# Kernel tuning notes

Measured on AMD Instinct MI355X. Metric: run time of the kernel, lower is better.

The kernel has to match this reference:

```python
import jax, jax.numpy as jnp
import numpy as np

N_NODES = 50000
N_EDGES = 800000
IN_C, HID_C, OUT_C = 256, 256, 128


def gcn_conv(x, W, b, row, col, n_nodes):
    """PyG GCNConv: linear transform, symmetric-normalized aggregation, bias.
    row/col already include self-loops. Messages flow row -> col."""
    h = x @ W  # [N, out]
    deg = jax.ops.segment_sum(jnp.ones_like(col, dtype=h.dtype), col, num_segments=n_nodes)
    d_inv_sqrt = jnp.where(deg > 0, jax.lax.rsqrt(jnp.maximum(deg, 1e-12)), 0.0)
    norm = d_inv_sqrt[row] * d_inv_sqrt[col]  # [E]
    msg = h[row] * norm[:, None]              # gather + scale, [E, out]
    out = jax.ops.segment_sum(msg, col, num_segments=n_nodes)  # scatter-add
    return out + b


def setup_inputs() -> dict:
    key = jax.random.key(0)
    k_x, k_e, k_w1, k_w2 = jax.random.split(key, 4)
    x = jax.random.normal(k_x, (N_NODES, IN_C), dtype=jnp.float32)
    edge_index = jax.random.randint(k_e, (2, N_EDGES), 0, N_NODES, dtype=jnp.int64)
    # Glorot-style init for GCN weights, zeros bias (PyG default)
    s1 = float(np.sqrt(6.0 / (IN_C + HID_C)))
    s2 = float(np.sqrt(6.0 / (HID_C + OUT_C)))
    W1 = jax.random.uniform(k_w1, (IN_C, HID_C), dtype=jnp.float32, minval=-s1, maxval=s1)
    b1 = jnp.zeros((HID_C,), dtype=jnp.float32)
    W2 = jax.random.uniform(k_w2, (HID_C, OUT_C), dtype=jnp.float32, minval=-s2, maxval=s2)
    b2 = jnp.zeros((OUT_C,), dtype=jnp.float32)
    return {"x": x, "edge_index": edge_index, "W1": W1, "b1": b1, "W2": W2, "b2": b2}


def reference(x, edge_index, W1, b1, W2, b2):
    n = x.shape[0]
    # add self-loops (PyG GCNConv default add_self_loops=True)
    loops = jnp.arange(n, dtype=edge_index.dtype)
    row = jnp.concatenate([edge_index[0], loops])
    col = jnp.concatenate([edge_index[1], loops])
    h = gcn_conv(x, W1, b1, row, col, n)
    h = jax.nn.relu(h)  # dropout p=0.0 -> identity
    out = gcn_conv(h, W2, b2, row, col, n)
    return out
```

## Files before the change

### kernel.cpp

```cpp
#include <hip/hip_runtime.h>

#define NN 50000
#define NE 800000
#define IN_C 256
#define HID_C 256
#define OUT_C 128

typedef unsigned short u16;
typedef __attribute__((ext_vector_type(8))) short short8;
typedef __attribute__((ext_vector_type(8))) unsigned short ushort8;
typedef __attribute__((ext_vector_type(4))) float f32x4;

__device__ __forceinline__ u16 f2b(float f) {
  unsigned int u = __float_as_uint(f);
  return (u16)((u + 0x7FFFu + ((u >> 16) & 1u)) >> 16);
}
__device__ __forceinline__ float b2f(u16 s) {
  return __uint_as_float(((unsigned int)s) << 16);
}


__global__ __launch_bounds__(256) void convw_zero(const float* __restrict__ W1,
                                                  const float* __restrict__ W2,
                                                  u16* __restrict__ W1t,
                                                  u16* __restrict__ W2t,
                                                  int* __restrict__ cnt) {
  int b = blockIdx.x;
  if (b < 256) {
    int id = b * 256 + threadIdx.x;
    if (id < 256 * 256) {
      int n = id >> 8, k = id & 255;
      W1t[id] = f2b(W1[k * 256 + n]);
    }
    if (id < 128 * 256) {
      int n = id >> 8, k = id & 255;
      W2t[id] = f2b(W2[k * 128 + n]);
    }
  } else {
    int i = (b - 256) * 256 + threadIdx.x;
    if (i < NN) cnt[i] = 0;
  }
}


__global__ __launch_bounds__(256) void hist_kernel(const int* __restrict__ col,
                                                   int* __restrict__ cnt, int E) {
  int e = blockIdx.x * blockDim.x + threadIdx.x;
  if (e < E) atomicAdd(&cnt[col[e]], 1);
}

__global__ __launch_bounds__(256) void scan1_kernel(const int* __restrict__ cnt,
                                                    int* __restrict__ bsum, int n) {
  __shared__ int ws[4];
  int i = blockIdx.x * 256 + threadIdx.x;
  int lane = threadIdx.x & 63, wid = threadIdx.x >> 6;
  int v = (i < n) ? cnt[i] : 0;
#pragma unroll
  for (int off = 32; off > 0; off >>= 1) v += __shfl_down(v, off, 64);
  if (lane == 0) ws[wid] = v;
  __syncthreads();
  if (threadIdx.x == 0) bsum[blockIdx.x] = ws[0] + ws[1] + ws[2] + ws[3];
}

__global__ __launch_bounds__(256) void scan2_kernel(const int* __restrict__ bsum,
                                                    int* __restrict__ boff,
                                                    int* __restrict__ row_off,
                                                    int nb, int n) {
  __shared__ int wsum[4], wpre[5];
  int lane = threadIdx.x & 63, wid = threadIdx.x >> 6;
  int v = (threadIdx.x < nb) ? bsum[threadIdx.x] : 0;
  int s = v;
#pragma unroll
  for (int off = 1; off < 64; off <<= 1) {
    int t = __shfl_up(s, off, 64);
    if (lane >= off) s += t;
  }
  if (lane == 63) wsum[wid] = s;
  __syncthreads();
  if (threadIdx.x == 0) {
    int acc = 0;
#pragma unroll
    for (int w = 0; w < 4; ++w) { wpre[w] = acc; acc += wsum[w]; }
    wpre[4] = acc;
  }
  __syncthreads();
  if (threadIdx.x < nb) boff[threadIdx.x] = wpre[wid] + (s - v);
  if (threadIdx.x == 0) row_off[n] = wpre[4];
}

__global__ __launch_bounds__(256) void scan3_kernel(const int* __restrict__ cnt,
                                                    const int* __restrict__ boff,
                                                    int* __restrict__ row_off,
                                                    int* __restrict__ cursor,
                                                    float* __restrict__ dinv, int n) {
  __shared__ int wsum[4], wpre[4];
  int i = blockIdx.x * 256 + threadIdx.x;
  int lane = threadIdx.x & 63, wid = threadIdx.x >> 6;
  int v = (i < n) ? cnt[i] : 0;
  int s = v;
#pragma unroll
  for (int off = 1; off < 64; off <<= 1) {
    int t = __shfl_up(s, off, 64);
    if (lane >= off) s += t;
  }
  if (lane == 63) wsum[wid] = s;
  __syncthreads();
  if (threadIdx.x == 0) {
    int acc = 0;
#pragma unroll
    for (int w = 0; w < 4; ++w) { wpre[w] = acc; acc += wsum[w]; }
  }
  __syncthreads();
  if (i < n) {
    int off = boff[blockIdx.x] + wpre[wid] + (s - v);
    row_off[i] = off;
    cursor[i] = off;
    dinv[i] = rsqrtf((float)(v + 1));
  }
}


template <bool A_IS_F32>
__device__ __forceinline__ void gemm_body(const void* __restrict__ Ap,
                                          const u16* __restrict__ Bt,
                                          const float* __restrict__ dscale,
                                          u16* __restrict__ C, int M, int N,
                                          int bx, int by,
                                          u16 (&Asl)[2][5120], u16 (&Bsl)[2][5120]) {
  const int tid = threadIdx.x;
  const int row0 = by * 128;
  const int col0 = bx * 128;

  f32x4 acc[4][4] = {};

  const int seg = tid & 7;
  const int rb = tid >> 3;
  const int wave = tid >> 6, lane = tid & 63;
  const int wm = wave >> 1, wn = wave & 1;
  const int qr = lane & 15, quad = lane >> 4;

  float4 aF[4];
  ushort4 aU[4];
  ushort4 bR[4];

  auto load_tiles = [&](int k0) {
    if constexpr (A_IS_F32) {
      const float* A = (const float*)Ap;
#pragma unroll
      for (int i = 0; i < 4; ++i) {
        int gr = row0 + rb + i * 32;
        aF[i] = (gr < M) ? *(const float4*)&A[(size_t)gr * 256 + k0 + seg * 4]
                         : make_float4(0.f, 0.f, 0.f, 0.f);
      }
    } else {
      const u16* A = (const u16*)Ap;
#pragma unroll
      for (int i = 0; i < 4; ++i) {
        int gr = row0 + rb + i * 32;
        aU[i] = (gr < M) ? *(const ushort4*)&A[(size_t)gr * 256 + k0 + seg * 4]
                         : make_ushort4(0, 0, 0, 0);
      }
    }
#pragma unroll
    for (int i = 0; i < 4; ++i) {
      int n = rb + i * 32;
      bR[i] = *(const ushort4*)&Bt[(size_t)(col0 + n) * 256 + k0 + seg * 4];
    }
  };

  auto write_lds = [&](int buf) {
#pragma unroll
    for (int i = 0; i < 4; ++i) {
      int r = rb + i * 32;
      ushort4 u;
      if constexpr (A_IS_F32) {
        u.x = f2b(aF[i].x); u.y = f2b(aF[i].y);
        u.z = f2b(aF[i].z); u.w = f2b(aF[i].w);
      } else {
        u = aU[i];
      }
      *(ushort4*)&Asl[buf][r * 40 + seg * 4] = u;
      *(ushort4*)&Bsl[buf][r * 40 + seg * 4] = bR[i];
    }
  };

  load_tiles(0);
  write_lds(0);
  __syncthreads();

#pragma unroll
  for (int it = 0; it < 8; ++it) {
    const int cur = it & 1;
    if (it < 7) load_tiles((it + 1) * 32);

    short8 afr[4], bfr[4];
#pragma unroll
    for (int mt = 0; mt < 4; ++mt)
      afr[mt] = *(const short8*)&Asl[cur][(wm * 64 + mt * 16 + qr) * 40 + quad * 8];
#pragma unroll
    for (int nt = 0; nt < 4; ++nt)
      bfr[nt] = *(const short8*)&Bsl[cur][(wn * 64 + nt * 16 + qr) * 40 + quad * 8];
#pragma unroll
    for (int mt = 0; mt < 4; ++mt)
#pragma unroll
      for (int nt = 0; nt < 4; ++nt)
        acc[mt][nt] = __builtin_amdgcn_mfma_f32_16x16x32_bf16(afr[mt], bfr[nt], acc[mt][nt], 0, 0, 0);

    if (it < 7) {
      write_lds(1 - cur);
      __syncthreads();
    }
  }

#pragma unroll
  for (int mt = 0; mt < 4; ++mt) {
#pragma unroll
    for (int i = 0; i < 4; ++i) {
      int gr = row0 + wm * 64 + mt * 16 + quad * 4 + i;
      if (gr < M) {
        float sc = dscale[gr];
#pragma unroll
        for (int nt = 0; nt < 4; ++nt) {
          int gc = col0 + wn * 64 + nt * 16 + qr;
          C[(size_t)gr * N + gc] = f2b(acc[mt][nt][i] * sc);
        }
      }
    }
  }
}

template <bool A_IS_F32>
__global__ __launch_bounds__(256) void gemm_mfma(const void* __restrict__ Ap,
                                                 const u16* __restrict__ Bt,
                                                 const float* __restrict__ dscale,
                                                 u16* __restrict__ C, int M, int N) {
  __shared__ u16 Asl[2][5120];
  __shared__ u16 Bsl[2][5120];
  gemm_body<A_IS_F32>(Ap, Bt, dscale, C, M, N, blockIdx.x, blockIdx.y, Asl, Bsl);
}

__global__ __launch_bounds__(256) void gemm1_scatter(const float* __restrict__ x,
                                                     const u16* __restrict__ W1t,
                                                     const float* __restrict__ dinv,
                                                     u16* __restrict__ Hb, int M, int N,
                                                     int ngb,
                                                     const int* __restrict__ row,
                                                     const int* __restrict__ col,
                                                     int* __restrict__ cursor,
                                                     int* __restrict__ csr, int E) {
  __shared__ u16 Asl[2][5120];
  __shared__ u16 Bsl[2][5120];
  int b = blockIdx.x;
  if (b < ngb) {
    gemm_body<true>(x, W1t, dinv, Hb, M, N, b & 1, b >> 1, Asl, Bsl);
  } else {
    int e = (b - ngb) * 256 + threadIdx.x;
    if (e < E) {
      int c = col[e];
      int p = atomicAdd(&cursor[c], 1);
      csr[p] = row[e];
    }
  }
}


__global__ __launch_bounds__(256) void agg256_bf(const u16* __restrict__ h,
                                                 const int* __restrict__ row_off,
                                                 const int* __restrict__ csr,
                                                 const float* __restrict__ dinv,
                                                 const float* __restrict__ bias,
                                                 u16* __restrict__ out, int n) {
  int wave = threadIdx.x >> 6;
  int lane = threadIdx.x & 63;
  int half = lane >> 5;
  int sl = lane & 31;
  int v = blockIdx.x * 8 + wave * 2 + half;
  if (v >= n) return;
  int beg = row_off[v], end = row_off[v + 1];
  float a[8] = {};
  int e = beg;
  for (; e < end && (e & 3); ++e) {
    int s0 = csr[e];
    ushort8 g0 = *(const ushort8*)&h[(size_t)s0 * 256 + sl * 8];
#pragma unroll
    for (int i = 0; i < 8; ++i) a[i] += b2f((u16)g0[i]);
  }
  for (; e + 7 < end; e += 8) {
    int4 i0 = *(const int4*)&csr[e];
    int4 i1 = *(const int4*)&csr[e + 4];
    int s[8] = {i0.x, i0.y, i0.z, i0.w, i1.x, i1.y, i1.z, i1.w};
    ushort8 g[8];
#pragma unroll
    for (int j = 0; j < 8; ++j)
      g[j] = *(const ushort8*)&h[(size_t)s[j] * 256 + sl * 8];
#pragma unroll
    for (int j = 0; j < 8; ++j)
#pragma unroll
      for (int i = 0; i < 8; ++i) a[i] += b2f((u16)g[j][i]);
  }
  for (; e < end; ++e) {
    int s0 = csr[e];
    ushort8 g0 = *(const ushort8*)&h[(size_t)s0 * 256 + sl * 8];
#pragma unroll
    for (int i = 0; i < 8; ++i) a[i] += b2f((u16)g0[i]);
  }
  ushort8 hs = *(const ushort8*)&h[(size_t)v * 256 + sl * 8];
#pragma unroll
  for (int i = 0; i < 8; ++i) a[i] += b2f((u16)hs[i]);
  float dv = dinv[v];
  float4 bv0 = *(const float4*)&bias[sl * 8];
  float4 bv1 = *(const float4*)&bias[sl * 8 + 4];
  float bb[8] = {bv0.x, bv0.y, bv0.z, bv0.w, bv1.x, bv1.y, bv1.z, bv1.w};
  ushort8 o;
#pragma unroll
  for (int i = 0; i < 8; ++i) {
    float r = fmaxf(a[i] * dv + bb[i], 0.f);
    o[i] = (short)f2b(r);
  }
  *(ushort8*)&out[(size_t)v * 256 + sl * 8] = o;
}

__global__ __launch_bounds__(256) void agg128_bf(const u16* __restrict__ h,
                                                 const int* __restrict__ row_off,
                                                 const int* __restrict__ csr,
                                                 const float* __restrict__ dinv,
                                                 const float* __restrict__ bias,
                                                 float* __restrict__ out, int n) {
  int wave = threadIdx.x >> 6;
  int lane = threadIdx.x & 63;
  int quarter = lane >> 4;
  int sl = lane & 15;
  int v = blockIdx.x * 16 + wave * 4 + quarter;
  if (v >= n) return;
  int beg = row_off[v], end = row_off[v + 1];
  float a[8] = {};
  int e = beg;
  for (; e < end && (e & 3); ++e) {
    int s0 = csr[e];
    ushort8 g0 = *(const ushort8*)&h[(size_t)s0 * 128 + sl * 8];
#pragma unroll
    for (int i = 0; i < 8; ++i) a[i] += b2f((u16)g0[i]);
  }
  for (; e + 7 < end; e += 8) {
    int4 i0 = *(const int4*)&csr[e];
    int4 i1 = *(const int4*)&csr[e + 4];
    int s[8] = {i0.x, i0.y, i0.z, i0.w, i1.x, i1.y, i1.z, i1.w};
    ushort8 g[8];
#pragma unroll
    for (int j = 0; j < 8; ++j)
      g[j] = *(const ushort8*)&h[(size_t)s[j] * 128 + sl * 8];
#pragma unroll
    for (int j = 0; j < 8; ++j)
#pragma unroll
      for (int i = 0; i < 8; ++i) a[i] += b2f((u16)g[j][i]);
  }
  for (; e < end; ++e) {
    int s0 = csr[e];
    ushort8 g0 = *(const ushort8*)&h[(size_t)s0 * 128 + sl * 8];
#pragma unroll
    for (int i = 0; i < 8; ++i) a[i] += b2f((u16)g0[i]);
  }
  ushort8 hs = *(const ushort8*)&h[(size_t)v * 128 + sl * 8];
#pragma unroll
  for (int i = 0; i < 8; ++i) a[i] += b2f((u16)hs[i]);
  float dv = dinv[v];
  float4 bv0 = *(const float4*)&bias[sl * 8];
  float4 bv1 = *(const float4*)&bias[sl * 8 + 4];
  float bb[8] = {bv0.x, bv0.y, bv0.z, bv0.w, bv1.x, bv1.y, bv1.z, bv1.w};
  float o[8];
#pragma unroll
  for (int i = 0; i < 8; ++i) o[i] = a[i] * dv + bb[i];
  *(float4*)&out[(size_t)v * 128 + sl * 8] = make_float4(o[0], o[1], o[2], o[3]);
  *(float4*)&out[(size_t)v * 128 + sl * 8 + 4] = make_float4(o[4], o[5], o[6], o[7]);
}


extern "C" void kernel_launch(void* const* d_in, const int* in_sizes, int n_in,
                              void* d_out, int out_size, void* d_ws, size_t ws_size,
                              hipStream_t stream) {
  const float* x = (const float*)d_in[0];
  const int* ei = (const int*)d_in[1];
  const float* W1 = (const float*)d_in[2];
  const float* b1 = (const float*)d_in[3];
  const float* W2 = (const float*)d_in[4];
  const float* b2 = (const float*)d_in[5];
  float* out = (float*)d_out;

  const int* row = ei;
  const int* col = ei + NE;

  const int NB = (NN + 255) / 256;

  u16* Hb = (u16*)d_ws;
  u16* H2b = Hb + (size_t)NN * 256;
  u16* H3b = H2b + (size_t)NN * 256;
  u16* W1t = H3b + (size_t)NN * 128;
  u16* W2t = W1t + 256 * 256;
  int* cnt = (int*)(W2t + 128 * 256);
  int* row_off = cnt + NN;
  int* cursor = row_off + NN + 4;
  float* dinv = (float*)(cursor + NN);
  int* bsum = (int*)(dinv + NN);
  int* boff = bsum + 200;
  int* csr = boff + 200;

  convw_zero<<<256 + NB, 256, 0, stream>>>(W1, W2, W1t, W2t, cnt);
  hist_kernel<<<(NE + 255) / 256, 256, 0, stream>>>(col, cnt, NE);
  scan1_kernel<<<NB, 256, 0, stream>>>(cnt, bsum, NN);
  scan2_kernel<<<1, 256, 0, stream>>>(bsum, boff, row_off, NB, NN);
  scan3_kernel<<<NB, 256, 0, stream>>>(cnt, boff, row_off, cursor, dinv, NN);

  {
    const int ngb = (HID_C / 128) * ((NN + 127) / 128);
    const int nsb = (NE + 255) / 256;
    gemm1_scatter<<<ngb + nsb, 256, 0, stream>>>(x, W1t, dinv, Hb, NN, HID_C, ngb,
                                                 row, col, cursor, csr, NE);
  }
  agg256_bf<<<(NN + 7) / 8, 256, 0, stream>>>(Hb, row_off, csr, dinv, b1, H2b, NN);

  {
    dim3 grid(OUT_C / 128, (NN + 127) / 128);
    gemm_mfma<false><<<grid, 256, 0, stream>>>(H2b, W2t, dinv, H3b, NN, OUT_C);
  }
  agg128_bf<<<(NN + 15) / 16, 256, 0, stream>>>(H3b, row_off, csr, dinv, b2, out, NN);
}
```

Baseline: 303.6 us.

## Overlap degree histogram with GEMM1 and store per-edge norm weights in CSR

Result: slower. 313.3 us (+3.2%).

```diff
diff --git a/kernel.cpp b/kernel.cpp
--- a/kernel.cpp
+++ b/kernel.cpp
@@ -43,12 +43,6 @@
 }
 
 
-__global__ __launch_bounds__(256) void hist_kernel(const int* __restrict__ col,
-                                                   int* __restrict__ cnt, int E) {
-  int e = blockIdx.x * blockDim.x + threadIdx.x;
-  if (e < E) atomicAdd(&cnt[col[e]], 1);
-}
-
 __global__ __launch_bounds__(256) void scan1_kernel(const int* __restrict__ cnt,
                                                     int* __restrict__ bsum, int n) {
   __shared__ int ws[4];
@@ -120,10 +114,29 @@
 }
 
 
+__global__ __launch_bounds__(256) void scatter_kernel(const int* __restrict__ row,
+                                                      const int* __restrict__ col,
+                                                      const float* __restrict__ dinv,
+                                                      int* __restrict__ cursor,
+                                                      int2* __restrict__ csr,
+                                                      int E, int T) {
+  int idx = blockIdx.x * 256 + threadIdx.x;
+#pragma unroll
+  for (int i = 0; i < 8; ++i) {
+    int e = idx + i * T;
+    if (e < E) {
+      int r = row[e], c = col[e];
+      float w = dinv[r] * dinv[c];
+      int p = atomicAdd(&cursor[c], 1);
+      csr[p] = make_int2(r, __float_as_int(w));
+    }
+  }
+}
+
+
 template <bool A_IS_F32>
 __device__ __forceinline__ void gemm_body(const void* __restrict__ Ap,
                                           const u16* __restrict__ Bt,
-                                          const float* __restrict__ dscale,
                                           u16* __restrict__ C, int M, int N,
                                           int bx, int by,
                                           u16 (&Asl)[2][5120], u16 (&Bsl)[2][5120]) {
@@ -215,15 +228,12 @@
 #pragma unroll
   for (int mt = 0; mt < 4; ++mt) {
 #pragma unroll
-    for (int i = 0; i < 4; ++i) {
-      int gr = row0 + wm * 64 + mt * 16 + quad * 4 + i;
-      if (gr < M) {
-        float sc = dscale[gr];
-#pragma unroll
-        for (int nt = 0; nt < 4; ++nt) {
-          int gc = col0 + wn * 64 + nt * 16 + qr;
-          C[(size_t)gr * N + gc] = f2b(acc[mt][nt][i] * sc);
-        }
+    for (int nt = 0; nt < 4; ++nt) {
+      int gc = col0 + wn * 64 + nt * 16 + qr;
+#pragma unroll
+      for (int i = 0; i < 4; ++i) {
+        int gr = row0 + wm * 64 + mt * 16 + quad * 4 + i;
+        if (gr < M) C[(size_t)gr * N + gc] = f2b(acc[mt][nt][i]);
       }
     }
   }
@@ -232,33 +242,30 @@
 template <bool A_IS_F32>
 __global__ __launch_bounds__(256) void gemm_mfma(const void* __restrict__ Ap,
                                                  const u16* __restrict__ Bt,
-                                                 const float* __restrict__ dscale,
                                                  u16* __restrict__ C, int M, int N) {
   __shared__ u16 Asl[2][5120];
   __shared__ u16 Bsl[2][5120];
-  gemm_body<A_IS_F32>(Ap, Bt, dscale, C, M, N, blockIdx.x, blockIdx.y, Asl, Bsl);
-}
-
-__global__ __launch_bounds__(256) void gemm1_scatter(const float* __restrict__ x,
-                                                     const u16* __restrict__ W1t,
-                                                     const float* __restrict__ dinv,
-                                                     u16* __restrict__ Hb, int M, int N,
-                                                     int ngb,
-                                                     const int* __restrict__ row,
-                                                     const int* __restrict__ col,
-                                                     int* __restrict__ cursor,
-                                                     int* __restrict__ csr, int E) {
+  gemm_body<A_IS_F32>(Ap, Bt, C, M, N, blockIdx.x, blockIdx.y, Asl, Bsl);
+}
+
+__global__ __launch_bounds__(256) void gemm1_hist(const float* __restrict__ x,
+                                                  const u16* __restrict__ W1t,
+                                                  u16* __restrict__ Hb, int M, int N,
+                                                  int ngb,
+                                                  const int* __restrict__ col,
+                                                  int* __restrict__ cnt, int E, int nhb) {
   __shared__ u16 Asl[2][5120];
   __shared__ u16 Bsl[2][5120];
   int b = blockIdx.x;
   if (b < ngb) {
-    gemm_body<true>(x, W1t, dinv, Hb, M, N, b & 1, b >> 1, Asl, Bsl);
+    gemm_body<true>(x, W1t, Hb, M, N, b & 1, b >> 1, Asl, Bsl);
   } else {
-    int e = (b - ngb) * 256 + threadIdx.x;
-    if (e < E) {
-      int c = col[e];
-      int p = atomicAdd(&cursor[c], 1);
-      csr[p] = row[e];
+    int T = nhb * 256;
+    int idx = (b - ngb) * 256 + threadIdx.x;
+#pragma unroll
+    for (int i = 0; i < 8; ++i) {
+      int e = idx + i * T;
+      if (e < E) atomicAdd(&cnt[col[e]], 1);
     }
   }
 }
@@ -266,7 +273,7 @@
 
 __global__ __launch_bounds__(256) void agg256_bf(const u16* __restrict__ h,
                                                  const int* __restrict__ row_off,
-                                                 const int* __restrict__ csr,
+                                                 const int2* __restrict__ csr,
                                                  const float* __restrict__ dinv,
                                                  const float* __restrict__ bias,
                                                  u16* __restrict__ out, int n) {
@@ -279,16 +286,24 @@
   int beg = row_off[v], end = row_off[v + 1];
   float a[8] = {};
   int e = beg;
-  for (; e < end && (e & 3); ++e) {
-    int s0 = csr[e];
-    ushort8 g0 = *(const ushort8*)&h[(size_t)s0 * 256 + sl * 8];
-#pragma unroll
-    for (int i = 0; i < 8; ++i) a[i] += b2f((u16)g0[i]);
+  if (e < end && (e & 1)) {
+    int2 e0 = csr[e];
+    ushort8 g0 = *(const ushort8*)&h[(size_t)e0.x * 256 + sl * 8];
+    float w0 = __int_as_float(e0.y);
+#pragma unroll
+    for (int i = 0; i < 8; ++i) a[i] += b2f((u16)g0[i]) * w0;
+    ++e;
   }
   for (; e + 7 < end; e += 8) {
-    int4 i0 = *(const int4*)&csr[e];
-    int4 i1 = *(const int4*)&csr[e + 4];
-    int s[8] = {i0.x, i0.y, i0.z, i0.w, i1.x, i1.y, i1.z, i1.w};
+    int4 p0 = *(const int4*)&csr[e];
+    int4 p1 = *(const int4*)&csr[e + 2];
+    int4 p2 = *(const int4*)&csr[e + 4];
+    int4 p3 = *(const int4*)&csr[e + 6];
+    int s[8] = {p0.x, p0.z, p1.x, p1.z, p2.x, p2.z, p3.x, p3.z};
+    float w[8] = {__int_as_float(p0.y), __int_as_float(p0.w),
+                  __int_as_float(p1.y), __int_as_float(p1.w),
+                  __int_as_float(p2.y), __int_as_float(p2.w),
+                  __int_as_float(p3.y), __int_as_float(p3.w)};
     ushort8 g[8];
 #pragma unroll
     for (int j = 0; j < 8; ++j)
@@ -296,25 +311,25 @@
 #pragma unroll
     for (int j = 0; j < 8; ++j)
 #pragma unroll
-      for (int i = 0; i < 8; ++i) a[i] += b2f((u16)g[j][i]);
+      for (int i = 0; i < 8; ++i) a[i] += b2f((u16)g[j][i]) * w[j];
   }
   for (; e < end; ++e) {
-    int s0 = csr[e];
-    ushort8 g0 = *(const ushort8*)&h[(size_t)s0 * 256 + sl * 8];
-#pragma unroll
-    for (int i = 0; i < 8; ++i) a[i] += b2f((u16)g0[i]);
-  }
+    int2 e0 = csr[e];
+    ushort8 g0 = *(const ushort8*)&h[(size_t)e0.x * 256 + sl * 8];
+    float w0 = __int_as_float(e0.y);
+#pragma unroll
+    for (int i = 0; i < 8; ++i) a[i] += b2f((u16)g0[i]) * w0;
+  }
+  float dv = dinv[v];
+  float sw = dv * dv;
   ushort8 hs = *(const ushort8*)&h[(size_t)v * 256 + sl * 8];
-#pragma unroll
-  for (int i = 0; i < 8; ++i) a[i] += b2f((u16)hs[i]);
-  float dv = dinv[v];
   float4 bv0 = *(const float4*)&bias[sl * 8];
   float4 bv1 = *(const float4*)&bias[sl * 8 + 4];
   float bb[8] = {bv0.x, bv0.y, bv0.z, bv0.w, bv1.x, bv1.y, bv1.z, bv1.w};
   ushort8 o;
 #pragma unroll
   for (int i = 0; i < 8; ++i) {
-    float r = fmaxf(a[i] * dv + bb[i], 0.f);
+    float r = fmaxf(a[i] + b2f((u16)hs[i]) * sw + bb[i], 0.f);
     o[i] = (short)f2b(r);
   }
   *(ushort8*)&out[(size_t)v * 256 + sl * 8] = o;
@@ -322,7 +337,7 @@
 
 __global__ __launch_bounds__(256) void agg128_bf(const u16* __restrict__ h,
                                                  const int* __restrict__ row_off,
-                                                 const int* __restrict__ csr,
+                                                 const int2* __restrict__ csr,
                                                  const float* __restrict__ dinv,
                                                  const float* __restrict__ bias,
                                                  float* __restrict__ out, int n) {
@@ -335,16 +350,24 @@
   int beg = row_off[v], end = row_off[v + 1];
   float a[8] = {};
   int e = beg;
-  for (; e < end && (e & 3); ++e) {
-    int s0 = csr[e];
-    ushort8 g0 = *(const ushort8*)&h[(size_t)s0 * 128 + sl * 8];
-#pragma unroll
-    for (int i = 0; i < 8; ++i) a[i] += b2f((u16)g0[i]);
+  if (e < end && (e & 1)) {
+    int2 e0 = csr[e];
+    ushort8 g0 = *(const ushort8*)&h[(size_t)e0.x * 128 + sl * 8];
+    float w0 = __int_as_float(e0.y);
+#pragma unroll
+    for (int i = 0; i < 8; ++i) a[i] += b2f((u16)g0[i]) * w0;
+    ++e;
   }
   for (; e + 7 < end; e += 8) {
-    int4 i0 = *(const int4*)&csr[e];
-    int4 i1 = *(const int4*)&csr[e + 4];
-    int s[8] = {i0.x, i0.y, i0.z, i0.w, i1.x, i1.y, i1.z, i1.w};
+    int4 p0 = *(const int4*)&csr[e];
+    int4 p1 = *(const int4*)&csr[e + 2];
+    int4 p2 = *(const int4*)&csr[e + 4];
+    int4 p3 = *(const int4*)&csr[e + 6];
+    int s[8] = {p0.x, p0.z, p1.x, p1.z, p2.x, p2.z, p3.x, p3.z};
+    float w[8] = {__int_as_float(p0.y), __int_as_float(p0.w),
+                  __int_as_float(p1.y), __int_as_float(p1.w),
+                  __int_as_float(p2.y), __int_as_float(p2.w),
+                  __int_as_float(p3.y), __int_as_float(p3.w)};
     ushort8 g[8];
 #pragma unroll
     for (int j = 0; j < 8; ++j)
@@ -352,24 +375,24 @@
 #pragma unroll
     for (int j = 0; j < 8; ++j)
 #pragma unroll
-      for (int i = 0; i < 8; ++i) a[i] += b2f((u16)g[j][i]);
+      for (int i = 0; i < 8; ++i) a[i] += b2f((u16)g[j][i]) * w[j];
   }
   for (; e < end; ++e) {
-    int s0 = csr[e];
-    ushort8 g0 = *(const ushort8*)&h[(size_t)s0 * 128 + sl * 8];
-#pragma unroll
-    for (int i = 0; i < 8; ++i) a[i] += b2f((u16)g0[i]);
-  }
+    int2 e0 = csr[e];
+    ushort8 g0 = *(const ushort8*)&h[(size_t)e0.x * 128 + sl * 8];
+    float w0 = __int_as_float(e0.y);
+#pragma unroll
+    for (int i = 0; i < 8; ++i) a[i] += b2f((u16)g0[i]) * w0;
+  }
+  float dv = dinv[v];
+  float sw = dv * dv;
   ushort8 hs = *(const ushort8*)&h[(size_t)v * 128 + sl * 8];
-#pragma unroll
-  for (int i = 0; i < 8; ++i) a[i] += b2f((u16)hs[i]);
-  float dv = dinv[v];
   float4 bv0 = *(const float4*)&bias[sl * 8];
   float4 bv1 = *(const float4*)&bias[sl * 8 + 4];
   float bb[8] = {bv0.x, bv0.y, bv0.z, bv0.w, bv1.x, bv1.y, bv1.z, bv1.w};
   float o[8];
 #pragma unroll
-  for (int i = 0; i < 8; ++i) o[i] = a[i] * dv + bb[i];
+  for (int i = 0; i < 8; ++i) o[i] = a[i] + b2f((u16)hs[i]) * sw + bb[i];
   *(float4*)&out[(size_t)v * 128 + sl * 8] = make_float4(o[0], o[1], o[2], o[3]);
   *(float4*)&out[(size_t)v * 128 + sl * 8 + 4] = make_float4(o[4], o[5], o[6], o[7]);
 }
@@ -402,25 +425,31 @@
   float* dinv = (float*)(cursor + NN);
   int* bsum = (int*)(dinv + NN);
   int* boff = bsum + 200;
-  int* csr = boff + 200;
+  int2* csr = (int2*)(boff + 200);
 
   convw_zero<<<256 + NB, 256, 0, stream>>>(W1, W2, W1t, W2t, cnt);
-  hist_kernel<<<(NE + 255) / 256, 256, 0, stream>>>(col, cnt, NE);
+
+  {
+    const int ngb = (HID_C / 128) * ((NN + 127) / 128);
+    const int nhb = (NE + 8 * 256 - 1) / (8 * 256);
+    gemm1_hist<<<ngb + nhb, 256, 0, stream>>>(x, W1t, Hb, NN, HID_C, ngb,
+                                              col, cnt, NE, nhb);
+  }
+
   scan1_kernel<<<NB, 256, 0, stream>>>(cnt, bsum, NN);
   scan2_kernel<<<1, 256, 0, stream>>>(bsum, boff, row_off, NB, NN);
   scan3_kernel<<<NB, 256, 0, stream>>>(cnt, boff, row_off, cursor, dinv, NN);
 
   {
-    const int ngb = (HID_C / 128) * ((NN + 127) / 128);
-    const int nsb = (NE + 255) / 256;
-    gemm1_scatter<<<ngb + nsb, 256, 0, stream>>>(x, W1t, dinv, Hb, NN, HID_C, ngb,
-                                                 row, col, cursor, csr, NE);
-  }
+    const int nsb = (NE + 8 * 256 - 1) / (8 * 256);
+    scatter_kernel<<<nsb, 256, 0, stream>>>(row, col, dinv, cursor, csr, NE, nsb * 256);
+  }
+
   agg256_bf<<<(NN + 7) / 8, 256, 0, stream>>>(Hb, row_off, csr, dinv, b1, H2b, NN);
 
   {
     dim3 grid(OUT_C / 128, (NN + 127) / 128);
-    gemm_mfma<false><<<grid, 256, 0, stream>>>(H2b, W2t, dinv, H3b, NN, OUT_C);
+    gemm_mfma<false><<<grid, 256, 0, stream>>>(H2b, W2t, H3b, NN, OUT_C);
   }
   agg128_bf<<<(NN + 15) / 16, 256, 0, stream>>>(H3b, row_off, csr, dinv, b2, out, NN);
 }
```

## Fuse histogram into weight conversion, merge scan passes, batch edges per thread

Applied to the files above, without the earlier changes.

Result: no change. 304.1 us (+0.2%).

```diff
diff --git a/kernel.cpp b/kernel.cpp
--- a/kernel.cpp
+++ b/kernel.cpp
@@ -20,34 +20,29 @@
 }
 
 
-__global__ __launch_bounds__(256) void convw_zero(const float* __restrict__ W1,
+__global__ __launch_bounds__(256) void convw_hist(const float* __restrict__ W1,
                                                   const float* __restrict__ W2,
                                                   u16* __restrict__ W1t,
                                                   u16* __restrict__ W2t,
-                                                  int* __restrict__ cnt) {
+                                                  const int* __restrict__ col,
+                                                  int* __restrict__ cnt, int E, int nhb) {
   int b = blockIdx.x;
   if (b < 256) {
     int id = b * 256 + threadIdx.x;
-    if (id < 256 * 256) {
-      int n = id >> 8, k = id & 255;
-      W1t[id] = f2b(W1[k * 256 + n]);
-    }
-    if (id < 128 * 256) {
-      int n = id >> 8, k = id & 255;
-      W2t[id] = f2b(W2[k * 128 + n]);
-    }
+    int n = id >> 8, k = id & 255;
+    W1t[id] = f2b(W1[k * 256 + n]);
+    if (id < 128 * 256) W2t[id] = f2b(W2[k * 128 + n]);
   } else {
-    int i = (b - 256) * 256 + threadIdx.x;
-    if (i < NN) cnt[i] = 0;
-  }
-}
-
-
-__global__ __launch_bounds__(256) void hist_kernel(const int* __restrict__ col,
-                                                   int* __restrict__ cnt, int E) {
-  int e = blockIdx.x * blockDim.x + threadIdx.x;
-  if (e < E) atomicAdd(&cnt[col[e]], 1);
-}
+    int T = nhb * 256;
+    int idx = (b - 256) * 256 + threadIdx.x;
+#pragma unroll
+    for (int i = 0; i < 8; ++i) {
+      int e = idx + i * T;
+      if (e < E) atomicAdd(&cnt[col[e]], 1);
+    }
+  }
+}
+
 
 __global__ __launch_bounds__(256) void scan1_kernel(const int* __restrict__ cnt,
                                                     int* __restrict__ bsum, int n) {
@@ -62,61 +57,45 @@
   if (threadIdx.x == 0) bsum[blockIdx.x] = ws[0] + ws[1] + ws[2] + ws[3];
 }
 
-__global__ __launch_bounds__(256) void scan2_kernel(const int* __restrict__ bsum,
-                                                    int* __restrict__ boff,
-                                                    int* __restrict__ row_off,
-                                                    int nb, int n) {
-  __shared__ int wsum[4], wpre[5];
-  int lane = threadIdx.x & 63, wid = threadIdx.x >> 6;
-  int v = (threadIdx.x < nb) ? bsum[threadIdx.x] : 0;
+__global__ __launch_bounds__(256) void scan23_kernel(const int* __restrict__ cnt,
+                                                     const int* __restrict__ bsum,
+                                                     int* __restrict__ row_off,
+                                                     int* __restrict__ cursor,
+                                                     float* __restrict__ dinv, int n) {
+  __shared__ int ws2[4];
+  __shared__ int wsum[4], wpre[4];
+  int bid = blockIdx.x;
+  int t = threadIdx.x;
+  int lane = t & 63, wid = t >> 6;
+  int bv = (t < bid) ? bsum[t] : 0;
+#pragma unroll
+  for (int off = 32; off > 0; off >>= 1) bv += __shfl_down(bv, off, 64);
+  if (lane == 0) ws2[wid] = bv;
+  __syncthreads();
+  int boff = ws2[0] + ws2[1] + ws2[2] + ws2[3];
+  int i = bid * 256 + t;
+  int v = (i < n) ? cnt[i] : 0;
   int s = v;
 #pragma unroll
   for (int off = 1; off < 64; off <<= 1) {
-    int t = __shfl_up(s, off, 64);
-    if (lane >= off) s += t;
+    int tt = __shfl_up(s, off, 64);
+    if (lane >= off) s += tt;
   }
   if (lane == 63) wsum[wid] = s;
   __syncthreads();
-  if (threadIdx.x == 0) {
-    int acc = 0;
-#pragma unroll
-    for (int w = 0; w < 4; ++w) { wpre[w] = acc; acc += wsum[w]; }
-    wpre[4] = acc;
-  }
-  __syncthreads();
-  if (threadIdx.x < nb) boff[threadIdx.x] = wpre[wid] + (s - v);
-  if (threadIdx.x == 0) row_off[n] = wpre[4];
-}
-
-__global__ __launch_bounds__(256) void scan3_kernel(const int* __restrict__ cnt,
-                                                    const int* __restrict__ boff,
-                                                    int* __restrict__ row_off,
-                                                    int* __restrict__ cursor,
-                                                    float* __restrict__ dinv, int n) {
-  __shared__ int wsum[4], wpre[4];
-  int i = blockIdx.x * 256 + threadIdx.x;
-  int lane = threadIdx.x & 63, wid = threadIdx.x >> 6;
-  int v = (i < n) ? cnt[i] : 0;
-  int s = v;
-#pragma unroll
-  for (int off = 1; off < 64; off <<= 1) {
-    int t = __shfl_up(s, off, 64);
-    if (lane >= off) s += t;
-  }
-  if (lane == 63) wsum[wid] = s;
-  __syncthreads();
-  if (threadIdx.x == 0) {
+  if (t == 0) {
     int acc = 0;
 #pragma unroll
     for (int w = 0; w < 4; ++w) { wpre[w] = acc; acc += wsum[w]; }
   }
   __syncthreads();
   if (i < n) {
-    int off = boff[blockIdx.x] + wpre[wid] + (s - v);
+    int off = boff + wpre[wid] + (s - v);
     row_off[i] = off;
     cursor[i] = off;
     dinv[i] = rsqrtf((float)(v + 1));
   }
+  if (bid == 0 && t == 0) row_off[n] = NE;
 }
 
 
@@ -247,18 +226,23 @@
                                                      const int* __restrict__ row,
                                                      const int* __restrict__ col,
                                                      int* __restrict__ cursor,
-                                                     int* __restrict__ csr, int E) {
+                                                     int* __restrict__ csr, int E, int nsb) {
   __shared__ u16 Asl[2][5120];
   __shared__ u16 Bsl[2][5120];
   int b = blockIdx.x;
   if (b < ngb) {
     gemm_body<true>(x, W1t, dinv, Hb, M, N, b & 1, b >> 1, Asl, Bsl);
   } else {
-    int e = (b - ngb) * 256 + threadIdx.x;
-    if (e < E) {
-      int c = col[e];
-      int p = atomicAdd(&cursor[c], 1);
-      csr[p] = row[e];
+    int T = nsb * 256;
+    int idx = (b - ngb) * 256 + threadIdx.x;
+#pragma unroll
+    for (int i = 0; i < 8; ++i) {
+      int e = idx + i * T;
+      if (e < E) {
+        int c = col[e];
+        int p = atomicAdd(&cursor[c], 1);
+        csr[p] = row[e];
+      }
     }
   }
 }
@@ -401,21 +385,26 @@
   int* cursor = row_off + NN + 4;
   float* dinv = (float*)(cursor + NN);
   int* bsum = (int*)(dinv + NN);
-  int* boff = bsum + 200;
-  int* csr = boff + 200;
-
-  convw_zero<<<256 + NB, 256, 0, stream>>>(W1, W2, W1t, W2t, cnt);
-  hist_kernel<<<(NE + 255) / 256, 256, 0, stream>>>(col, cnt, NE);
+  int* boff_unused = bsum + 200;
+  int* csr = boff_unused + 200;
+
+  hipMemsetAsync(cnt, 0, NN * sizeof(int), stream);
+
+  {
+    const int nhb = (NE + 8 * 256 - 1) / (8 * 256);
+    convw_hist<<<256 + nhb, 256, 0, stream>>>(W1, W2, W1t, W2t, col, cnt, NE, nhb);
+  }
+
   scan1_kernel<<<NB, 256, 0, stream>>>(cnt, bsum, NN);
-  scan2_kernel<<<1, 256, 0, stream>>>(bsum, boff, row_off, NB, NN);
-  scan3_kernel<<<NB, 256, 0, stream>>>(cnt, boff, row_off, cursor, dinv, NN);
+  scan23_kernel<<<NB, 256, 0, stream>>>(cnt, bsum, row_off, cursor, dinv, NN);
 
   {
     const int ngb = (HID_C / 128) * ((NN + 127) / 128);
-    const int nsb = (NE + 255) / 256;
+    const int nsb = (NE + 8 * 256 - 1) / (8 * 256);
     gemm1_scatter<<<ngb + nsb, 256, 0, stream>>>(x, W1t, dinv, Hb, NN, HID_C, ngb,
-                                                 row, col, cursor, csr, NE);
-  }
+                                                 row, col, cursor, csr, NE, nsb);
+  }
+
   agg256_bf<<<(NN + 7) / 8, 256, 0, stream>>>(Hb, row_off, csr, dinv, b1, H2b, NN);
 
   {
```
